# Kernel tuning notes

Hardware: AMD Instinct MI355X
Metric: run time of the kernel (lower is better)

The kernel has to match this reference:

```python
import jax, jax.numpy as jnp
import numpy as np

B, L, D = 32, 128, 48          # batch, time steps, features
R = 64                          # no_reference_time_point
INIT_TIME, MAX_TS = 0.0, 48.0   # linspace bounds for reference time points


def setup_inputs() -> dict:
    key = jax.random.key(0)
    ks = jax.random.split(key, 10)
    def glorot(k, shape):
        fan_in = int(np.prod(shape[:-1])) if len(shape) > 1 else shape[0]
        fan_out = shape[-1]
        lim = float(np.sqrt(6.0 / (fan_in + fan_out)))
        return jax.random.uniform(k, shape, jnp.float32, -lim, lim)
    return {
        "X": jax.random.normal(ks[0], (B, L, D), jnp.float32),
        "T": jax.random.uniform(ks[1], (B, L, D), jnp.float32) * MAX_TS,
        "M": jax.random.uniform(ks[2], (B, L, D), jnp.float32),
        "DT": jax.random.uniform(ks[3], (B, L, D), jnp.float32),
        "P": jax.random.normal(ks[4], (B, L, D), jnp.float32),
        "alpha": glorot(ks[5], (R, 1, 1)),
        "w_t": glorot(ks[6], (R, L, D, 5)),
        "b_t": glorot(ks[7], (R, L, D, 1)),
        "w_v": glorot(ks[8], (R, L, D)),
        "b_v": glorot(ks[9], (R, 1, D)),
    }


def reference(X, T, M, DT, P, alpha, w_t, b_t, w_v, b_v) -> jnp.ndarray:
    # reference time points: [R,1,1]
    ref = jnp.linspace(INIT_TIME, MAX_TS, R, dtype=jnp.float32).reshape(R, 1, 1)
    # broadcast inputs over reference axis: [B,R,L,D]
    t = T[:, None, :, :]
    dist = jnp.abs(t - ref)                         # type_distance == 'abs'
    kernel = jnp.exp(-jax.nn.relu(alpha) * dist)    # [B,R,L,D]
    x = X[:, None, :, :] * jnp.ones((1, R, 1, 1), jnp.float32)
    intensity = jax.nn.relu(x * kernel)             # [B,R,L,D]
    # stack the 5 channels: [B,R,L,D,5]
    c = jnp.stack(
        [x,
         intensity,
         jnp.broadcast_to(M[:, None, :, :], x.shape),
         jnp.broadcast_to(DT[:, None, :, :], x.shape),
         jnp.broadcast_to(P[:, None, :, :], x.shape)],
        axis=-1)
    # temporal projection: sum over channel axis (b_t broadcast over the 5 channels)
    h = jax.nn.relu(jnp.sum(w_t * c + b_t, axis=-1))       # [B,R,L,D]
    # value projection: sum over time-step axis L (b_v [R,1,D] broadcast over L)
    out = jax.nn.relu(jnp.sum(w_v * h + b_v, axis=2))       # [B,R,D]
    return out
```

## Files before the change

kernel.cpp:

```cpp
#include <hip/hip_runtime.h>
#include <hip/hip_bf16.h>

#define PB 32
#define PL 128
#define PD 48
#define PR 64

__global__ __launch_bounds__(256) void alnn_kernel(
    const float* __restrict__ X,
    const float* __restrict__ T,
    const float* __restrict__ M,
    const float* __restrict__ DT,
    const float* __restrict__ P,
    const float* __restrict__ alpha,
    const float* __restrict__ w_t,
    const float* __restrict__ b_t,
    const float* __restrict__ w_v,
    const float* __restrict__ b_v,
    float* __restrict__ out)
{
    const int bid = blockIdx.x;
    const int r = bid & (PR - 1);
    const int b = bid >> 6;
    const int t = threadIdx.x;
    const int lg = t >> 6;
    const int d  = t & 63;

    __shared__ float part[4][PD];

    float ar = alpha[r];
    ar = ar > 0.0f ? ar : 0.0f;
    const float refr = 48.0f * (float)r / 63.0f;

    float acc = 0.0f;
    if (d < PD) {
        const int in_base = b * (PL * PD);
        const int wt_base = r * (PL * PD * 5);
        const int rv_base = r * (PL * PD);
        #pragma unroll 4
        for (int li = 0; li < 32; ++li) {
            const int l  = lg * 32 + li;
            const int id = in_base + l * PD + d;
            const float x  = X[id];
            const float tt = T[id];
            const float m  = M[id];
            const float dt = DT[id];
            const float p  = P[id];

            const float dist = fabsf(tt - refr);
            const float kern = __expf(-ar * dist);
            float inten = x * kern;
            inten = inten > 0.0f ? inten : 0.0f;

            const int wi = wt_base + l * (PD * 5) + d * 5;
            const int vi = rv_base + l * PD + d;
            float h = w_t[wi + 0] * x
                    + w_t[wi + 1] * inten
                    + w_t[wi + 2] * m
                    + w_t[wi + 3] * dt
                    + w_t[wi + 4] * p
                    + 5.0f * b_t[vi];
            h = h > 0.0f ? h : 0.0f;

            acc += w_v[vi] * h;
        }
        part[lg][d] = acc;
    }
    __syncthreads();

    if (lg == 0 && d < PD) {
        float s = part[0][d] + part[1][d] + part[2][d] + part[3][d]
                + 128.0f * b_v[r * PD + d];
        s = s > 0.0f ? s : 0.0f;
        out[b * (PR * PD) + r * PD + d] = s;
    }
}

extern "C" void kernel_launch(void* const* d_in, const int* in_sizes, int n_in,
                              void* d_out, int out_size, void* d_ws, size_t ws_size,
                              hipStream_t stream) {
    const float* X     = (const float*)d_in[0];
    const float* T     = (const float*)d_in[1];
    const float* M     = (const float*)d_in[2];
    const float* DT    = (const float*)d_in[3];
    const float* P     = (const float*)d_in[4];
    const float* alpha = (const float*)d_in[5];
    const float* w_t   = (const float*)d_in[6];
    const float* b_t   = (const float*)d_in[7];
    const float* w_v   = (const float*)d_in[8];
    const float* b_v   = (const float*)d_in[9];
    float* out = (float*)d_out;

    alnn_kernel<<<PB * PR, 256, 0, stream>>>(X, T, M, DT, P, alpha, w_t, b_t, w_v, b_v, out);
}
```

Before: 109.9 us.

## Vectorize loads with float4 and remap threads to 4 features each

Each thread now handles 4 consecutive features, using float4 loads for inputs, w_t (5 float4s), b_t and w_v. The block shrinks to 192 threads so no lanes sit idle (the old layout left 16 of every 64 lanes unused), and the time axis is split across 16 groups reduced through shared memory. This targets load instruction count and wasted lanes, at the cost of more registers and a longer final reduction.

```diff
diff --git a/kernel.cpp b/kernel.cpp
--- a/kernel.cpp
+++ b/kernel.cpp
@@ -6,7 +6,7 @@
 #define PD 48
 #define PR 64
 
-__global__ __launch_bounds__(256) void alnn_kernel(
+__global__ __launch_bounds__(192) void alnn_kernel(
     const float* __restrict__ X,
     const float* __restrict__ T,
     const float* __restrict__ M,
@@ -22,57 +22,86 @@
     const int bid = blockIdx.x;
     const int r = bid & (PR - 1);
     const int b = bid >> 6;
-    const int t = threadIdx.x;
-    const int lg = t >> 6;
-    const int d  = t & 63;
+    const int tid = threadIdx.x;
+    const int lg = tid / 12;
+    const int dq = tid - lg * 12;
 
-    __shared__ float part[4][PD];
+    __shared__ float4 part[16][12];
 
     float ar = alpha[r];
     ar = ar > 0.0f ? ar : 0.0f;
     const float refr = 48.0f * (float)r / 63.0f;
 
-    float acc = 0.0f;
-    if (d < PD) {
-        const int in_base = b * (PL * PD);
-        const int wt_base = r * (PL * PD * 5);
-        const int rv_base = r * (PL * PD);
-        #pragma unroll 4
-        for (int li = 0; li < 32; ++li) {
-            const int l  = lg * 32 + li;
-            const int id = in_base + l * PD + d;
-            const float x  = X[id];
-            const float tt = T[id];
-            const float m  = M[id];
-            const float dt = DT[id];
-            const float p  = P[id];
+    const int in_base = b * (PL * PD) + dq * 4;
+    const int wt_base = r * (PL * PD * 5) + dq * 20;
+    const int rv_base = r * (PL * PD) + dq * 4;
 
-            const float dist = fabsf(tt - refr);
+    float acc[4] = {0.0f, 0.0f, 0.0f, 0.0f};
+
+    #pragma unroll
+    for (int li = 0; li < 8; ++li) {
+        const int l = li * 16 + lg;
+        const int io = in_base + l * PD;
+        const float4 x4  = *(const float4*)(X  + io);
+        const float4 t4  = *(const float4*)(T  + io);
+        const float4 m4  = *(const float4*)(M  + io);
+        const float4 dt4 = *(const float4*)(DT + io);
+        const float4 p4  = *(const float4*)(P  + io);
+
+        const float* wp = w_t + wt_base + l * (PD * 5);
+        float w[20];
+        *(float4*)(w +  0) = *(const float4*)(wp +  0);
+        *(float4*)(w +  4) = *(const float4*)(wp +  4);
+        *(float4*)(w +  8) = *(const float4*)(wp +  8);
+        *(float4*)(w + 12) = *(const float4*)(wp + 12);
+        *(float4*)(w + 16) = *(const float4*)(wp + 16);
+
+        const int vo = rv_base + l * PD;
+        const float4 bt4 = *(const float4*)(b_t + vo);
+        const float4 wv4 = *(const float4*)(w_v + vo);
+
+        const float xs[4]  = {x4.x,  x4.y,  x4.z,  x4.w};
+        const float ts[4]  = {t4.x,  t4.y,  t4.z,  t4.w};
+        const float ms[4]  = {m4.x,  m4.y,  m4.z,  m4.w};
+        const float dts[4] = {dt4.x, dt4.y, dt4.z, dt4.w};
+        const float ps[4]  = {p4.x,  p4.y,  p4.z,  p4.w};
+        const float bts[4] = {bt4.x, bt4.y, bt4.z, bt4.w};
+        const float wvs[4] = {wv4.x, wv4.y, wv4.z, wv4.w};
+
+        #pragma unroll
+        for (int j = 0; j < 4; ++j) {
+            const float x = xs[j];
+            const float dist = fabsf(ts[j] - refr);
             const float kern = __expf(-ar * dist);
             float inten = x * kern;
             inten = inten > 0.0f ? inten : 0.0f;
+            float h = w[j*5 + 0] * x
+                    + w[j*5 + 1] * inten
+                    + w[j*5 + 2] * ms[j]
+                    + w[j*5 + 3] * dts[j]
+                    + w[j*5 + 4] * ps[j]
+                    + 5.0f * bts[j];
+            h = h > 0.0f ? h : 0.0f;
+            acc[j] += wvs[j] * h;
+        }
+    }
 
-            const int wi = wt_base + l * (PD * 5) + d * 5;
-            const int vi = rv_base + l * PD + d;
-            float h = w_t[wi + 0] * x
-                    + w_t[wi + 1] * inten
-                    + w_t[wi + 2] * m
-                    + w_t[wi + 3] * dt
-                    + w_t[wi + 4] * p
-                    + 5.0f * b_t[vi];
-            h = h > 0.0f ? h : 0.0f;
-
-            acc += w_v[vi] * h;
-        }
-        part[lg][d] = acc;
-    }
+    part[lg][dq] = make_float4(acc[0], acc[1], acc[2], acc[3]);
     __syncthreads();
 
-    if (lg == 0 && d < PD) {
-        float s = part[0][d] + part[1][d] + part[2][d] + part[3][d]
-                + 128.0f * b_v[r * PD + d];
-        s = s > 0.0f ? s : 0.0f;
-        out[b * (PR * PD) + r * PD + d] = s;
+    if (tid < 12) {
+        float4 s = part[0][tid];
+        #pragma unroll
+        for (int g = 1; g < 16; ++g) {
+            const float4 q = part[g][tid];
+            s.x += q.x; s.y += q.y; s.z += q.z; s.w += q.w;
+        }
+        const float4 bv4 = *(const float4*)(b_v + r * PD + tid * 4);
+        s.x = fmaxf(s.x + 128.0f * bv4.x, 0.0f);
+        s.y = fmaxf(s.y + 128.0f * bv4.y, 0.0f);
+        s.z = fmaxf(s.z + 128.0f * bv4.z, 0.0f);
+        s.w = fmaxf(s.w + 128.0f * bv4.w, 0.0f);
+        *(float4*)(out + b * (PR * PD) + r * PD + tid * 4) = s;
     }
 }
 
@@ -91,5 +120,5 @@
     const float* b_v   = (const float*)d_in[9];
     float* out = (float*)d_out;
 
-    alnn_kernel<<<PB * PR, 256, 0, stream>>>(X, T, M, DT, P, alpha, w_t, b_t, w_v, b_v, out);
+    alnn_kernel<<<PB * PR, 192, 0, stream>>>(X, T, M, DT, P, alpha, w_t, b_t, w_v, b_v, out);
 }
```

After: 109.0 us. No clear change (-0.8%).
